# Performance work log

Hardware: AMD Instinct MI355X
Metric: run time of the kernel (lower is better)

## Reference

```python
import jax, jax.numpy as jnp
import numpy as np

DIST_THD = 2.0  # squared-distance threshold from my_chamfer_fn


def setup_inputs() -> dict:
    key = jax.random.key(0)
    k1, k2 = jax.random.split(key)
    pc1 = jax.random.normal(k1, (1, 16384, 3), dtype=jnp.float32)
    pc2 = jax.random.normal(k2, (1, 16384, 3), dtype=jnp.float32)
    return {"pc1": pc1, "pc2": pc2}


def _chamfer(x, y):
    # x: (N, P1, D), y: (N, P2, D). Squared pairwise distances (as pytorch3d knn_points).
    x2 = jnp.sum(x * x, axis=-1)                       # (N, P1)
    y2 = jnp.sum(y * y, axis=-1)                       # (N, P2)
    xy = jnp.einsum('npd,nqd->npq', x, y)              # (N, P1, P2)
    d2 = x2[:, :, None] + y2[:, None, :] - 2.0 * xy    # (N, P1, P2)
    cham_x = jnp.min(d2, axis=2)                       # (N, P1) NN dist x->y (K=1)
    cham_y = jnp.min(d2, axis=1)                       # (N, P2) NN dist y->x
    # threshold mask: distances >= 2 are zeroed
    cham_x = jnp.where(cham_x >= DIST_THD, 0.0, cham_x)
    cham_y = jnp.where(cham_y >= DIST_THD, 0.0, cham_y)
    N, P1, _ = x.shape
    P2 = y.shape[1]
    # point_reduction='mean' (lengths are full P), batch_reduction='mean'
    cx = jnp.sum(cham_x, axis=1) / P1
    cy = jnp.sum(cham_y, axis=1) / P2
    return jnp.sum(cx) / N + jnp.sum(cy) / N


def reference(pc1, pc2):
    # Chamfer loss between pc1 and pc2 (the kernel inside NSFP optimization);
    # normals are unused in this code path, so only the distance loss is returned.
    return _chamfer(pc1, pc2)
```

## Files before the change

### kernel.cpp

```cpp
#include <hip/hip_runtime.h>
#include <hip/hip_bf16.h>


constexpr int P      = 16384;
constexpr int BLK    = 256;
constexpr int XPT    = 16;
constexpr int XCHUNK = BLK * XPT;
constexpr int YSPLIT = 64;
constexpr int YSEG   = P / YSPLIT;
constexpr int NGRP   = YSEG / 2;

typedef float v2f __attribute__((ext_vector_type(2)));

static __device__ inline v2f pk_fma(v2f a, v2f b, v2f c) {
    v2f d;
    asm("v_pk_fma_f32 %0, %1, %2, %3" : "=v"(d) : "v"(a), "v"(b), "v"(c));
    return d;
}
static __device__ inline float max3(float a, float b, float c) {
    float d;
    asm("v_max3_f32 %0, %1, %2, %3" : "=v"(d) : "v"(a), "v"(b), "v"(c));
    return d;
}

__global__ __launch_bounds__(BLK, 2) void chamfer_main(
    const float* __restrict__ pc1, const float* __restrict__ pc2,
    float* __restrict__ partial,
    float* __restrict__ out)
{
    if (blockIdx.x == 0 && blockIdx.y == 0 && blockIdx.z == 0 && threadIdx.x == 0)
        out[0] = 0.0f;

    const int dir = blockIdx.z;
    const float* xs = dir ? pc2 : pc1;
    const float* ys = dir ? pc1 : pc2;

    __shared__ __align__(16) float yt[NGRP * 8];
    {
        const int j = threadIdx.x;
        const int q = blockIdx.y * YSEG + j;
        const float a = ys[3 * q], b = ys[3 * q + 1], c = ys[3 * q + 2];
        const float w = -0.5f * fmaf(a, a, fmaf(b, b, c * c));
        const float a2 = __shfl_xor(a, 1, 64);
        const float b2 = __shfl_xor(b, 1, 64);
        const float c2 = __shfl_xor(c, 1, 64);
        const float w2 = __shfl_xor(w, 1, 64);
        const float4 v = (j & 1) ? make_float4(c2, c, w2, w)
                                 : make_float4(a, a2, b, b2);
        ((float4*)yt)[j] = v;
    }

    const int p0 = blockIdx.x * XCHUNK + threadIdx.x;
    v2f xs0[XPT], xs1[XPT], xs2[XPT];
    float acc[XPT];
    #pragma unroll
    for (int k = 0; k < XPT; ++k) {
        const int p = p0 + k * BLK;
        const float a = xs[3 * p], b = xs[3 * p + 1], c = xs[3 * p + 2];
        xs0[k] = (v2f){a, a};
        xs1[k] = (v2f){b, b};
        xs2[k] = (v2f){c, c};
        acc[k] = -3.0e38f;
    }
    __syncthreads();

    const float4* gptr = (const float4*)yt;
    #pragma unroll 2
    for (int g = 0; g < NGRP; ++g) {
        const float4 A = gptr[2 * g];
        const float4 B = gptr[2 * g + 1];
        const v2f y0 = {A.x, A.y};
        const v2f y1 = {A.z, A.w};
        const v2f y2 = {B.x, B.y};
        const v2f yw = {B.z, B.w};
        #pragma unroll
        for (int k = 0; k < XPT; ++k) {
            v2f t = pk_fma(xs0[k], y0, yw);
            t = pk_fma(xs1[k], y1, t);
            t = pk_fma(xs2[k], y2, t);
            acc[k] = max3(acc[k], t.x, t.y);
        }
    }

    float* pout = partial + ((size_t)dir * YSPLIT + blockIdx.y) * P;
    #pragma unroll
    for (int k = 0; k < XPT; ++k) pout[p0 + k * BLK] = acc[k];
}

__global__ __launch_bounds__(BLK) void chamfer_reduce(
    const float* __restrict__ partial,
    const float* __restrict__ pc1, const float* __restrict__ pc2,
    float* __restrict__ out)
{
    const int gid = blockIdx.x * BLK + threadIdx.x;
    const int dir = (gid >= P) ? 1 : 0;
    const int p = gid & (P - 1);
    const float* xsrc = dir ? pc2 : pc1;
    const float* base = partial + (size_t)dir * YSPLIT * P + p;

    float M = base[0];
    #pragma unroll
    for (int s = 1; s < YSPLIT; ++s) M = fmaxf(M, base[(size_t)s * P]);

    const float a = xsrc[3 * p], b = xsrc[3 * p + 1], c = xsrc[3 * p + 2];
    const float xx = fmaf(a, a, fmaf(b, b, c * c));
    float d2 = fmaf(-2.0f, M, xx);
    if (d2 >= 2.0f) d2 = 0.0f;
    float v = d2 * (1.0f / (float)P);

    #pragma unroll
    for (int off = 32; off > 0; off >>= 1) v += __shfl_down(v, off, 64);

    __shared__ float wsum[BLK / 64];
    const int lane = threadIdx.x & 63;
    const int wv = threadIdx.x >> 6;
    if (lane == 0) wsum[wv] = v;
    __syncthreads();
    if (threadIdx.x == 0) {
        float s = wsum[0];
        #pragma unroll
        for (int w = 1; w < BLK / 64; ++w) s += wsum[w];
        atomicAdd(out, s);
    }
}

extern "C" void kernel_launch(void* const* d_in, const int* in_sizes, int n_in,
                              void* d_out, int out_size, void* d_ws, size_t ws_size,
                              hipStream_t stream) {
    const float* pc1 = (const float*)d_in[0];
    const float* pc2 = (const float*)d_in[1];
    float* out = (float*)d_out;
    float* partial = (float*)d_ws;

    dim3 grid(P / XCHUNK, YSPLIT, 2);
    chamfer_main<<<grid, BLK, 0, stream>>>(pc1, pc2, partial, out);
    chamfer_reduce<<<(2 * P) / BLK, BLK, 0, stream>>>(partial, pc1, pc2, out);
}
```

Baseline: 102.1 us.

## Pack x coordinates with op_sel, raise occupancy, double y-split, prefetch LDS

Stores each x point's coordinates packed into fewer VGPRs and uses v_pk_fma op_sel modifiers to broadcast the needed half, cutting x register usage from six to three floats per point. Launch bounds rise to four blocks per CU. The y dimension is split into 128 segments when the workspace allows, giving a larger grid of shorter blocks. The next LDS group is software-prefetched each iteration. The tradeoffs are twice the partial buffer size and more reduce-kernel reads, and the occupancy target may force register spills.

Result: slower. 124.0 us (+21.4%).

```diff
diff --git a/kernel.cpp b/kernel.cpp
--- a/kernel.cpp
+++ b/kernel.cpp
@@ -6,15 +6,19 @@
 constexpr int BLK    = 256;
 constexpr int XPT    = 16;
 constexpr int XCHUNK = BLK * XPT;
-constexpr int YSPLIT = 64;
-constexpr int YSEG   = P / YSPLIT;
-constexpr int NGRP   = YSEG / 2;
 
 typedef float v2f __attribute__((ext_vector_type(2)));
 
-static __device__ inline v2f pk_fma(v2f a, v2f b, v2f c) {
+static __device__ inline v2f pk_fma_lo(v2f xp, v2f y, v2f c) {
     v2f d;
-    asm("v_pk_fma_f32 %0, %1, %2, %3" : "=v"(d) : "v"(a), "v"(b), "v"(c));
+    asm("v_pk_fma_f32 %0, %1, %2, %3 op_sel:[0,0,0] op_sel_hi:[0,1,1]"
+        : "=v"(d) : "v"(xp), "v"(y), "v"(c));
+    return d;
+}
+static __device__ inline v2f pk_fma_hi(v2f xp, v2f y, v2f c) {
+    v2f d;
+    asm("v_pk_fma_f32 %0, %1, %2, %3 op_sel:[1,0,0] op_sel_hi:[1,1,1]"
+        : "=v"(d) : "v"(xp), "v"(y), "v"(c));
     return d;
 }
 static __device__ inline float max3(float a, float b, float c) {
@@ -23,11 +27,15 @@
     return d;
 }
 
-__global__ __launch_bounds__(BLK, 2) void chamfer_main(
+template <int YSPLIT>
+__global__ __launch_bounds__(BLK, 4) void chamfer_main(
     const float* __restrict__ pc1, const float* __restrict__ pc2,
     float* __restrict__ partial,
     float* __restrict__ out)
 {
+    constexpr int YSEG = P / YSPLIT;
+    constexpr int NGRP = YSEG / 2;
+
     if (blockIdx.x == 0 && blockIdx.y == 0 && blockIdx.z == 0 && threadIdx.x == 0)
         out[0] = 0.0f;
 
@@ -38,48 +46,54 @@
     __shared__ __align__(16) float yt[NGRP * 8];
     {
         const int j = threadIdx.x;
-        const int q = blockIdx.y * YSEG + j;
-        const float a = ys[3 * q], b = ys[3 * q + 1], c = ys[3 * q + 2];
-        const float w = -0.5f * fmaf(a, a, fmaf(b, b, c * c));
-        const float a2 = __shfl_xor(a, 1, 64);
-        const float b2 = __shfl_xor(b, 1, 64);
-        const float c2 = __shfl_xor(c, 1, 64);
-        const float w2 = __shfl_xor(w, 1, 64);
-        const float4 v = (j & 1) ? make_float4(c2, c, w2, w)
-                                 : make_float4(a, a2, b, b2);
-        ((float4*)yt)[j] = v;
+        if (j < YSEG) {
+            const int q = blockIdx.y * YSEG + j;
+            const float a = ys[3 * q], b = ys[3 * q + 1], c = ys[3 * q + 2];
+            const float w = -0.5f * fmaf(a, a, fmaf(b, b, c * c));
+            const float a2 = __shfl_xor(a, 1, 64);
+            const float b2 = __shfl_xor(b, 1, 64);
+            const float c2 = __shfl_xor(c, 1, 64);
+            const float w2 = __shfl_xor(w, 1, 64);
+            const float4 v = (j & 1) ? make_float4(c2, c, w2, w)
+                                     : make_float4(a, a2, b, b2);
+            ((float4*)yt)[j] = v;
+        }
     }
 
     const int p0 = blockIdx.x * XCHUNK + threadIdx.x;
-    v2f xs0[XPT], xs1[XPT], xs2[XPT];
+    v2f xa[XPT];
+    v2f xb[XPT / 2];
     float acc[XPT];
     #pragma unroll
     for (int k = 0; k < XPT; ++k) {
         const int p = p0 + k * BLK;
         const float a = xs[3 * p], b = xs[3 * p + 1], c = xs[3 * p + 2];
-        xs0[k] = (v2f){a, a};
-        xs1[k] = (v2f){b, b};
-        xs2[k] = (v2f){c, c};
+        xa[k] = (v2f){a, b};
+        if (k & 1) xb[k >> 1].y = c; else xb[k >> 1].x = c;
         acc[k] = -3.0e38f;
     }
     __syncthreads();
 
     const float4* gptr = (const float4*)yt;
+    float4 A = gptr[0], B = gptr[1];
     #pragma unroll 2
     for (int g = 0; g < NGRP; ++g) {
-        const float4 A = gptr[2 * g];
-        const float4 B = gptr[2 * g + 1];
+        const int gn = (2 * g + 2) & (2 * NGRP - 1);
+        const float4 An = gptr[gn];
+        const float4 Bn = gptr[gn + 1];
         const v2f y0 = {A.x, A.y};
         const v2f y1 = {A.z, A.w};
         const v2f y2 = {B.x, B.y};
         const v2f yw = {B.z, B.w};
         #pragma unroll
         for (int k = 0; k < XPT; ++k) {
-            v2f t = pk_fma(xs0[k], y0, yw);
-            t = pk_fma(xs1[k], y1, t);
-            t = pk_fma(xs2[k], y2, t);
+            v2f t = pk_fma_lo(xa[k], y0, yw);
+            t = pk_fma_hi(xa[k], y1, t);
+            t = (k & 1) ? pk_fma_hi(xb[k >> 1], y2, t)
+                        : pk_fma_lo(xb[k >> 1], y2, t);
             acc[k] = max3(acc[k], t.x, t.y);
         }
+        A = An; B = Bn;
     }
 
     float* pout = partial + ((size_t)dir * YSPLIT + blockIdx.y) * P;
@@ -87,6 +101,7 @@
     for (int k = 0; k < XPT; ++k) pout[p0 + k * BLK] = acc[k];
 }
 
+template <int YSPLIT>
 __global__ __launch_bounds__(BLK) void chamfer_reduce(
     const float* __restrict__ partial,
     const float* __restrict__ pc1, const float* __restrict__ pc2,
@@ -99,7 +114,7 @@
     const float* base = partial + (size_t)dir * YSPLIT * P + p;
 
     float M = base[0];
-    #pragma unroll
+    #pragma unroll 8
     for (int s = 1; s < YSPLIT; ++s) M = fmaxf(M, base[(size_t)s * P]);
 
     const float a = xsrc[3 * p], b = xsrc[3 * p + 1], c = xsrc[3 * p + 2];
@@ -132,7 +147,13 @@
     float* out = (float*)d_out;
     float* partial = (float*)d_ws;
 
-    dim3 grid(P / XCHUNK, YSPLIT, 2);
-    chamfer_main<<<grid, BLK, 0, stream>>>(pc1, pc2, partial, out);
-    chamfer_reduce<<<(2 * P) / BLK, BLK, 0, stream>>>(partial, pc1, pc2, out);
+    if (ws_size >= (size_t)2 * 128 * P * sizeof(float)) {
+        dim3 grid(P / XCHUNK, 128, 2);
+        chamfer_main<128><<<grid, BLK, 0, stream>>>(pc1, pc2, partial, out);
+        chamfer_reduce<128><<<(2 * P) / BLK, BLK, 0, stream>>>(partial, pc1, pc2, out);
+    } else {
+        dim3 grid(P / XCHUNK, 64, 2);
+        chamfer_main<64><<<grid, BLK, 0, stream>>>(pc1, pc2, partial, out);
+        chamfer_reduce<64><<<(2 * P) / BLK, BLK, 0, stream>>>(partial, pc1, pc2, out);
+    }
 }
```
